# Kernel optimization log

Hardware: AMD Instinct MI355X
Metric: run time of the kernel (lower is better)

## Reference

```python
import jax, jax.numpy as jnp
import numpy as np

B, T, E = 4, 2048, 1024
H, KV = 16, 4          # query heads, key/value heads
D = E // H             # head_dim = 64
G = H // KV            # query heads per kv head = 4
NEG = -1e9


def setup_inputs() -> dict:
    key = jax.random.key(0)
    ks = jax.random.split(key, 6)
    hidden_states = jax.random.normal(ks[0], (B, T, E), dtype=jnp.float32)
    # additive causal mask [B, 1, T, T]
    causal = jnp.where(jnp.tril(jnp.ones((T, T), dtype=bool)), 0.0, NEG).astype(jnp.float32)
    attention_mask = jnp.broadcast_to(causal[None, None], (B, 1, T, T))
    s = 0.02
    Wq = jax.random.normal(ks[1], (E, E), dtype=jnp.float32) * s
    Wk = jax.random.normal(ks[2], (E, KV * D), dtype=jnp.float32) * s
    Wv = jax.random.normal(ks[3], (E, KV * D), dtype=jnp.float32) * s
    Wo = jax.random.normal(ks[4], (E, E), dtype=jnp.float32) * s
    bq = jnp.zeros((E,), jnp.float32)
    bk = jnp.zeros((KV * D,), jnp.float32)
    bv = jnp.zeros((KV * D,), jnp.float32)
    bo = jnp.zeros((E,), jnp.float32)
    return {"hidden_states": hidden_states, "attention_mask": attention_mask,
            "Wq": Wq, "bq": bq, "Wk": Wk, "bk": bk, "Wv": Wv, "bv": bv,
            "Wo": Wo, "bo": bo}


def reference(hidden_states, attention_mask, Wq, bq, Wk, bk, Wv, bv, Wo, bo):
    b, t, e = hidden_states.shape
    scaling = D ** -0.5
    # projections (torch Linear: x @ W + b with W stored [in, out])
    q = (hidden_states @ Wq + bq) * scaling           # [b, t, E]
    k = hidden_states @ Wk + bk                        # [b, t, KV*D]
    v = hidden_states @ Wv + bv
    # [b, KV, G, t, D] for q; [b, KV, t, D] for k/v (GQA grouping == repeat_kv math)
    q = q.reshape(b, t, KV, G, D).transpose(0, 2, 3, 1, 4)
    k = k.reshape(b, t, KV, D).transpose(0, 2, 1, 3)
    v = v.reshape(b, t, KV, D).transpose(0, 2, 1, 3)
    scores = jnp.einsum('bkgsd,bktd->bkgst', q, k)     # [b, KV, G, t, t]
    scores = scores + attention_mask[:, :, None, :, :]  # broadcast [b,1,1,t,t]
    w = jax.nn.softmax(scores, axis=-1)
    out = jnp.einsum('bkgst,bktd->bkgsd', w, v)        # [b, KV, G, t, D]
    out = out.transpose(0, 3, 1, 2, 4).reshape(b, t, e)  # heads back to embed
    return out @ Wo + bo
```

## Files before the change

kernel.cpp:

```cpp
#include <hip/hip_runtime.h>

typedef __bf16 bf16;
typedef __attribute__((ext_vector_type(8))) __bf16 bf16x8;
typedef __attribute__((ext_vector_type(4))) __bf16 bf16x4;
typedef __attribute__((ext_vector_type(4))) float f32x4;

#define B_ 4
#define T_ 2048
#define E_ 1024
#define H_ 16
#define KV_ 4
#define D_ 64
#define KVD_ 256
#define QKVS_ 1536
#define M_ 8192

#define MASK_NEG (-3.0e4f)
#define QSCALE (0.125f * 1.4426950408889634f)

__device__ inline bf16x8 load8(const bf16* p) { return *(const bf16x8*)p; }
__device__ inline bf16x8 load8(const float* p) {
  f32x4 a = *(const f32x4*)p;
  f32x4 b = *(const f32x4*)(p + 4);
  bf16x8 r;
#pragma unroll
  for (int j = 0; j < 4; ++j) { r[j] = (bf16)a[j]; r[4 + j] = (bf16)b[j]; }
  return r;
}

__device__ inline void gload_lds16(const bf16* g, bf16* l) {
  __builtin_amdgcn_global_load_lds(
      (const __attribute__((address_space(1))) void*)g,
      (__attribute__((address_space(3))) void*)l, 16, 0, 0);
}

__global__ __launch_bounds__(256) void prep_k(const float* __restrict__ hidden,
                                              bf16* __restrict__ Hb,
                                              const float* __restrict__ Wq,
                                              const float* __restrict__ Wk,
                                              const float* __restrict__ Wv,
                                              const float* __restrict__ Wo,
                                              bf16* __restrict__ WqkvT,
                                              bf16* __restrict__ WoT) {
  const int z = blockIdx.z;
  if (z >= 4) {
    size_t lin = (size_t)blockIdx.x + 32 * blockIdx.y + 1024 * (z - 4);
    size_t i = lin * 2048 + (size_t)threadIdx.x * 8;
    *(bf16x8*)(Hb + i) = load8(hidden + i);
    return;
  }
  const float* W;
  bf16* WT;
  int N;
  if (z == 0) { W = Wq; WT = WqkvT; N = 1024; }
  else if (z == 1) { W = Wo; WT = WoT; N = 1024; }
  else if (z == 2) { if (blockIdx.y >= 8) return; W = Wk; WT = WqkvT + 1024 * 1024; N = 256; }
  else { if (blockIdx.y >= 8) return; W = Wv; WT = WqkvT + 1280 * 1024; N = 256; }

  __shared__ bf16 tile[32][33];
  int k0 = blockIdx.x * 32, n0 = blockIdx.y * 32;
  int tr = threadIdx.x >> 5;
  int tc = threadIdx.x & 31;
#pragma unroll
  for (int i = 0; i < 32; i += 8)
    tile[tr + i][tc] = (bf16)W[(size_t)(k0 + tr + i) * N + n0 + tc];
  __syncthreads();
#pragma unroll
  for (int i = 0; i < 32; i += 8)
    WT[(size_t)(n0 + tr + i) * 1024 + k0 + tc] = tile[tc][tr + i];
}

__global__ __launch_bounds__(256) void vtrans_k(const bf16* __restrict__ src,
                                                bf16* __restrict__ dst) {
  __shared__ bf16 tile[32][33];
  int r0 = blockIdx.x * 32;
  int c0 = blockIdx.y * 32;
  int tr = threadIdx.x >> 5, tc = threadIdx.x & 31;
#pragma unroll
  for (int i = 0; i < 32; i += 8)
    tile[tr + i][tc] = src[(size_t)(r0 + tr + i) * QKVS_ + 1280 + c0 + tc];
  __syncthreads();
#pragma unroll
  for (int i = 0; i < 32; i += 8) {
    int c = c0 + tr + i;
    int r = r0 + tc;
    dst[(size_t)((r >> 11) * KVD_ + c) * T_ + (r & (T_ - 1))] = tile[tc][tr + i];
  }
}

__global__ __launch_bounds__(256) void qkv_gemm_k(const bf16* __restrict__ A,
                                                  const bf16* __restrict__ WT,
                                                  const float* __restrict__ bq,
                                                  const float* __restrict__ bk,
                                                  const float* __restrict__ bv,
                                                  bf16* __restrict__ C) {
  const int K = E_;
  const int m0 = blockIdx.x * 128;
  const int n0 = blockIdx.y * 128;
  const int tid = threadIdx.x;
  const int wave = tid >> 6;
  const int lane = tid & 63;
  const int wr = wave >> 1;
  const int wc = wave & 1;
  const int fr = lane & 15;
  const int quad = lane >> 4;

  __shared__ bf16 sA[128][32];
  __shared__ bf16 sB[128][32];

  f32x4 acc[4][4] = {};

  const int ldr = lane >> 2;
  const int ldk = (lane & 3) * 8;
  const bf16* Ag0 = A + (size_t)(m0 + wave * 32 + ldr) * K + ldk;
  const bf16* Ag1 = Ag0 + (size_t)16 * K;
  const bf16* Bg0 = WT + (size_t)(n0 + wave * 32 + ldr) * K + ldk;
  const bf16* Bg1 = Bg0 + (size_t)16 * K;
  bf16* sA0 = &sA[wave * 32][0];
  bf16* sA1 = &sA[wave * 32 + 16][0];
  bf16* sB0 = &sB[wave * 32][0];
  bf16* sB1 = &sB[wave * 32 + 16][0];

  for (int k0 = 0; k0 < K; k0 += 32) {
    gload_lds16(Ag0 + k0, sA0);
    gload_lds16(Ag1 + k0, sA1);
    gload_lds16(Bg0 + k0, sB0);
    gload_lds16(Bg1 + k0, sB1);
    __syncthreads();

    bf16x8 af[4], bfr[4];
#pragma unroll
    for (int m = 0; m < 4; ++m)
      af[m] = *(const bf16x8*)(&sA[wr * 64 + m * 16 + fr][quad * 8]);
#pragma unroll
    for (int n = 0; n < 4; ++n)
      bfr[n] = *(const bf16x8*)(&sB[wc * 64 + n * 16 + fr][quad * 8]);
#pragma unroll
    for (int m = 0; m < 4; ++m)
#pragma unroll
      for (int n = 0; n < 4; ++n)
        acc[m][n] = __builtin_amdgcn_mfma_f32_16x16x32_bf16(af[m], bfr[n], acc[m][n], 0, 0, 0);
    __syncthreads();
  }

#pragma unroll
  for (int n = 0; n < 4; ++n) {
    int col = n0 + wc * 64 + n * 16 + fr;
    float bias, sc;
    if (col < 1024) { bias = bq[col]; sc = QSCALE; }
    else if (col < 1280) { bias = bk[col - 1024]; sc = 1.f; }
    else { bias = bv[col - 1280]; sc = 1.f; }
#pragma unroll
    for (int m = 0; m < 4; ++m) {
#pragma unroll
      for (int i = 0; i < 4; ++i) {
        int row = m0 + wr * 64 + m * 16 + quad * 4 + i;
        C[(size_t)row * QKVS_ + col] = (bf16)((acc[m][n][i] + bias) * sc);
      }
    }
  }
}

__global__ __launch_bounds__(256) void gemm128_k(const bf16* __restrict__ A,
                                                 const bf16* __restrict__ WT,
                                                 const float* __restrict__ bias,
                                                 float* __restrict__ C,
                                                 int M, int N, int K) {
  const int m0 = blockIdx.x * 128;
  const int n0 = blockIdx.y * 128;
  const int tid = threadIdx.x;
  const int wave = tid >> 6;
  const int lane = tid & 63;
  const int wr = wave >> 1;
  const int wc = wave & 1;
  const int fr = lane & 15;
  const int quad = lane >> 4;

  __shared__ bf16 sA[128][32];
  __shared__ bf16 sB[128][32];

  f32x4 acc[4][4] = {};

  const int ldr = lane >> 2;
  const int ldk = (lane & 3) * 8;
  const bf16* Ag0 = A + (size_t)(m0 + wave * 32 + ldr) * K + ldk;
  const bf16* Ag1 = Ag0 + (size_t)16 * K;
  const bf16* Bg0 = WT + (size_t)(n0 + wave * 32 + ldr) * K + ldk;
  const bf16* Bg1 = Bg0 + (size_t)16 * K;
  bf16* sA0 = &sA[wave * 32][0];
  bf16* sA1 = &sA[wave * 32 + 16][0];
  bf16* sB0 = &sB[wave * 32][0];
  bf16* sB1 = &sB[wave * 32 + 16][0];

  for (int k0 = 0; k0 < K; k0 += 32) {
    gload_lds16(Ag0 + k0, sA0);
    gload_lds16(Ag1 + k0, sA1);
    gload_lds16(Bg0 + k0, sB0);
    gload_lds16(Bg1 + k0, sB1);
    __syncthreads();

    bf16x8 af[4], bfr[4];
#pragma unroll
    for (int m = 0; m < 4; ++m)
      af[m] = *(const bf16x8*)(&sA[wr * 64 + m * 16 + fr][quad * 8]);
#pragma unroll
    for (int n = 0; n < 4; ++n)
      bfr[n] = *(const bf16x8*)(&sB[wc * 64 + n * 16 + fr][quad * 8]);
#pragma unroll
    for (int m = 0; m < 4; ++m)
#pragma unroll
      for (int n = 0; n < 4; ++n)
        acc[m][n] = __builtin_amdgcn_mfma_f32_16x16x32_bf16(af[m], bfr[n], acc[m][n], 0, 0, 0);
    __syncthreads();
  }

#pragma unroll
  for (int n = 0; n < 4; ++n) {
    int col = n0 + wc * 64 + n * 16 + fr;
    float bv = bias[col];
#pragma unroll
    for (int m = 0; m < 4; ++m) {
#pragma unroll
      for (int i = 0; i < 4; ++i) {
        int row = m0 + wr * 64 + m * 16 + quad * 4 + i;
        C[(size_t)row * N + col] = (acc[m][n][i] + bv);
      }
    }
  }
}

__global__ __launch_bounds__(256) void attn_k(const bf16* __restrict__ QKVg,
                                              const bf16* __restrict__ VTg,
                                              bf16* __restrict__ Og) {
  const int jp = blockIdx.x;
  const int h = blockIdx.y;
  const int b = blockIdx.z;
  const int kv = h >> 2;
  const int tid = threadIdx.x;
  const int wave = tid >> 6;
  const int lane = tid & 63;
  const int fr = lane & 15;
  const int quad = lane >> 4;

  __shared__ bf16 Ks[64][72];
  __shared__ bf16 Vt[64][72];
  __shared__ bf16 Pt[64][72];

  const int skey = tid & 63;
  const int sdc = (tid >> 6) * 16;
  const int svd = tid >> 2;
  const int svk = (tid & 3) * 16;
  const bf16* kbase = QKVg + (size_t)(b * T_ + skey) * QKVS_ + 1024 + kv * 64 + sdc;
  const bf16* vbase = VTg + (size_t)((b * KV_ + kv) * D_ + svd) * T_ + svk;

  for (int ph = 0; ph < 2; ++ph) {
    const int qb = ph ? (31 - jp) : jp;

    bf16x8 qa0, qa1;
    {
      const bf16* qsrc = QKVg + (size_t)(b * T_ + qb * 64 + wave * 16 + fr) * QKVS_ + h * 64 + quad * 8;
      qa0 = *(const bf16x8*)(qsrc);
      qa1 = *(const bf16x8*)(qsrc + 32);
    }

    f32x4 Oacc[4] = {};
    float l_run = 0.f;

    bf16x8 k0p, k1p, v0p, v1p;
    k0p = *(const bf16x8*)(kbase);
    k1p = *(const bf16x8*)(kbase + 8);
    v0p = *(const bf16x8*)(vbase);
    v1p = *(const bf16x8*)(vbase + 8);

    for (int kb = 0; kb <= qb; ++kb) {
      *(bf16x8*)(&Ks[skey][sdc]) = k0p;
      *(bf16x8*)(&Ks[skey][sdc + 8]) = k1p;
      *(bf16x8*)(&Vt[svd][svk]) = v0p;
      *(bf16x8*)(&Vt[svd][svk + 8]) = v1p;
      __syncthreads();

      if (kb < qb) {
        const bf16* kp = kbase + (size_t)(kb + 1) * 64 * QKVS_;
        const bf16* vp = vbase + (size_t)(kb + 1) * 64;
        k0p = *(const bf16x8*)(kp);
        k1p = *(const bf16x8*)(kp + 8);
        v0p = *(const bf16x8*)(vp);
        v1p = *(const bf16x8*)(vp + 8);
      } else if (ph == 0) {
        k0p = *(const bf16x8*)(kbase);
        k1p = *(const bf16x8*)(kbase + 8);
        v0p = *(const bf16x8*)(vbase);
        v1p = *(const bf16x8*)(vbase + 8);
      }

      f32x4 S[4] = {};
      __builtin_amdgcn_s_setprio(1);
#pragma unroll
      for (int nt = 0; nt < 4; ++nt) {
        bf16x8 kf0 = *(const bf16x8*)(&Ks[nt * 16 + fr][quad * 8]);
        bf16x8 kf1 = *(const bf16x8*)(&Ks[nt * 16 + fr][32 + quad * 8]);
        S[nt] = __builtin_amdgcn_mfma_f32_16x16x32_bf16(kf0, qa0, S[nt], 0, 0, 0);
        S[nt] = __builtin_amdgcn_mfma_f32_16x16x32_bf16(kf1, qa1, S[nt], 0, 0, 0);
      }
      __builtin_amdgcn_s_setprio(0);

      if (kb == qb) {
        const int ql = wave * 16 + fr;
#pragma unroll
        for (int nt = 0; nt < 4; ++nt)
#pragma unroll
          for (int i = 0; i < 4; ++i)
            if (nt * 16 + quad * 4 + i > ql) S[nt][i] = MASK_NEG;
      }

      float ps = 0.f;
#pragma unroll
      for (int nt = 0; nt < 4; ++nt)
#pragma unroll
        for (int i = 0; i < 4; ++i) {
          float p = exp2f(S[nt][i]);
          S[nt][i] = p;
          ps += p;
        }
      ps += __shfl_xor(ps, 16, 64);
      ps += __shfl_xor(ps, 32, 64);
      l_run += ps;

#pragma unroll
      for (int nt = 0; nt < 4; ++nt) {
        bf16x4 w;
#pragma unroll
        for (int i = 0; i < 4; ++i) w[i] = (bf16)S[nt][i];
        *(bf16x4*)(&Pt[wave * 16 + fr][nt * 16 + quad * 4]) = w;
      }
      __threadfence_block();

      bf16x8 pb0 = *(const bf16x8*)(&Pt[wave * 16 + fr][quad * 8]);
      bf16x8 pb1 = *(const bf16x8*)(&Pt[wave * 16 + fr][32 + quad * 8]);
      __builtin_amdgcn_s_setprio(1);
#pragma unroll
      for (int dt = 0; dt < 4; ++dt) {
        bf16x8 vf0 = *(const bf16x8*)(&Vt[dt * 16 + fr][quad * 8]);
        bf16x8 vf1 = *(const bf16x8*)(&Vt[dt * 16 + fr][32 + quad * 8]);
        Oacc[dt] = __builtin_amdgcn_mfma_f32_16x16x32_bf16(vf0, pb0, Oacc[dt], 0, 0, 0);
        Oacc[dt] = __builtin_amdgcn_mfma_f32_16x16x32_bf16(vf1, pb1, Oacc[dt], 0, 0, 0);
      }
      __builtin_amdgcn_s_setprio(0);
      __syncthreads();
    }

    {
      float inv = 1.f / fmaxf(l_run, 1e-30f);
      bf16* dst = Og + (size_t)(b * T_ + qb * 64 + wave * 16 + fr) * E_ + h * 64;
#pragma unroll
      for (int dt = 0; dt < 4; ++dt) {
        bf16x4 o;
#pragma unroll
        for (int i = 0; i < 4; ++i) o[i] = (bf16)(Oacc[dt][i] * inv);
        *(bf16x4*)(dst + dt * 16 + quad * 4) = o;
      }
    }
  }
}

extern "C" void kernel_launch(void* const* d_in, const int* in_sizes, int n_in,
                              void* d_out, int out_size, void* d_ws, size_t ws_size,
                              hipStream_t stream) {
  (void)in_sizes; (void)n_in; (void)out_size; (void)ws_size;
  const float* hidden = (const float*)d_in[0];
  const float* Wq = (const float*)d_in[2];
  const float* bq = (const float*)d_in[3];
  const float* Wk = (const float*)d_in[4];
  const float* bk = (const float*)d_in[5];
  const float* Wv = (const float*)d_in[6];
  const float* bv = (const float*)d_in[7];
  const float* Wo = (const float*)d_in[8];
  const float* bo = (const float*)d_in[9];
  float* out = (float*)d_out;

  char* ws = (char*)d_ws;
  bf16* WqkvT = (bf16*)(ws);
  bf16* WoT   = (bf16*)(ws + (3u << 20));
  bf16* QKVb  = (bf16*)(ws + (5u << 20));
  bf16* Hb    = (bf16*)(ws + (29u << 20));
  bf16* Ab    = (bf16*)(ws + (29u << 20));
  bf16* VbT   = (bf16*)(ws + (45u << 20));

  prep_k<<<dim3(32, 32, 8), 256, 0, stream>>>(hidden, Hb, Wq, Wk, Wv, Wo, WqkvT, WoT);

  qkv_gemm_k<<<dim3(64, 12), 256, 0, stream>>>(Hb, WqkvT, bq, bk, bv, QKVb);

  vtrans_k<<<dim3(256, 8), 256, 0, stream>>>(QKVb, VbT);

  attn_k<<<dim3(16, 16, 4), 256, 0, stream>>>(QKVb, VbT, Ab);

  gemm128_k<<<dim3(64, 8), 256, 0, stream>>>(Ab, WoT, bo, out, M_, E_, E_);
}
```

Baseline: 278.4 us.

## Use two waves per attention block, each handling 32 query rows

The attention kernel drops from four waves of 256 threads to two waves of 128 threads, and each wave now processes two 16-row query subtiles. Every K and V fragment read from shared memory is reused across twice as many MFMAs, which cuts LDS read traffic and barrier participants per block. Each thread now stages 32 elements of K and V instead of 16, and register use rises from doubled accumulators and Q fragments. Fewer waves per block may lower the latency hiding available within a block.

```diff
diff --git a/kernel.cpp b/kernel.cpp
--- a/kernel.cpp
+++ b/kernel.cpp
@@ -229,7 +229,7 @@
   }
 }
 
-__global__ __launch_bounds__(256) void attn_k(const bf16* __restrict__ QKVg,
+__global__ __launch_bounds__(128) void attn_k(const bf16* __restrict__ QKVg,
                                               const bf16* __restrict__ VTg,
                                               bf16* __restrict__ Og) {
   const int jp = blockIdx.x;
@@ -247,36 +247,45 @@
   __shared__ bf16 Pt[64][72];
 
   const int skey = tid & 63;
-  const int sdc = (tid >> 6) * 16;
-  const int svd = tid >> 2;
-  const int svk = (tid & 3) * 16;
-  const bf16* kbase = QKVg + (size_t)(b * T_ + skey) * QKVS_ + 1024 + kv * 64 + sdc;
-  const bf16* vbase = VTg + (size_t)((b * KV_ + kv) * D_ + svd) * T_ + svk;
+  const int sseg = (tid >> 6) * 32;
+  const bf16* kbase = QKVg + (size_t)(b * T_ + skey) * QKVS_ + 1024 + kv * 64 + sseg;
+  const bf16* vbase = VTg + (size_t)((b * KV_ + kv) * D_ + skey) * T_ + sseg;
 
   for (int ph = 0; ph < 2; ++ph) {
     const int qb = ph ? (31 - jp) : jp;
 
-    bf16x8 qa0, qa1;
+    bf16x8 qa0, qa1, qc0, qc1;
     {
-      const bf16* qsrc = QKVg + (size_t)(b * T_ + qb * 64 + wave * 16 + fr) * QKVS_ + h * 64 + quad * 8;
+      const bf16* qsrc = QKVg + (size_t)(b * T_ + qb * 64 + wave * 32 + fr) * QKVS_ + h * 64 + quad * 8;
       qa0 = *(const bf16x8*)(qsrc);
       qa1 = *(const bf16x8*)(qsrc + 32);
+      const bf16* qsrc2 = qsrc + (size_t)16 * QKVS_;
+      qc0 = *(const bf16x8*)(qsrc2);
+      qc1 = *(const bf16x8*)(qsrc2 + 32);
     }
 
-    f32x4 Oacc[4] = {};
-    float l_run = 0.f;
-
-    bf16x8 k0p, k1p, v0p, v1p;
+    f32x4 O0[4] = {}, O1[4] = {};
+    float l0 = 0.f, l1 = 0.f;
+
+    bf16x8 k0p, k1p, k2p, k3p, v0p, v1p, v2p, v3p;
     k0p = *(const bf16x8*)(kbase);
     k1p = *(const bf16x8*)(kbase + 8);
+    k2p = *(const bf16x8*)(kbase + 16);
+    k3p = *(const bf16x8*)(kbase + 24);
     v0p = *(const bf16x8*)(vbase);
     v1p = *(const bf16x8*)(vbase + 8);
+    v2p = *(const bf16x8*)(vbase + 16);
+    v3p = *(const bf16x8*)(vbase + 24);
 
     for (int kb = 0; kb <= qb; ++kb) {
-      *(bf16x8*)(&Ks[skey][sdc]) = k0p;
-      *(bf16x8*)(&Ks[skey][sdc + 8]) = k1p;
-      *(bf16x8*)(&Vt[svd][svk]) = v0p;
-      *(bf16x8*)(&Vt[svd][svk + 8]) = v1p;
+      *(bf16x8*)(&Ks[skey][sseg]) = k0p;
+      *(bf16x8*)(&Ks[skey][sseg + 8]) = k1p;
+      *(bf16x8*)(&Ks[skey][sseg + 16]) = k2p;
+      *(bf16x8*)(&Ks[skey][sseg + 24]) = k3p;
+      *(bf16x8*)(&Vt[skey][sseg]) = v0p;
+      *(bf16x8*)(&Vt[skey][sseg + 8]) = v1p;
+      *(bf16x8*)(&Vt[skey][sseg + 16]) = v2p;
+      *(bf16x8*)(&Vt[skey][sseg + 24]) = v3p;
       __syncthreads();
 
       if (kb < qb) {
@@ -284,80 +293,111 @@
         const bf16* vp = vbase + (size_t)(kb + 1) * 64;
         k0p = *(const bf16x8*)(kp);
         k1p = *(const bf16x8*)(kp + 8);
+        k2p = *(const bf16x8*)(kp + 16);
+        k3p = *(const bf16x8*)(kp + 24);
         v0p = *(const bf16x8*)(vp);
         v1p = *(const bf16x8*)(vp + 8);
+        v2p = *(const bf16x8*)(vp + 16);
+        v3p = *(const bf16x8*)(vp + 24);
       } else if (ph == 0) {
         k0p = *(const bf16x8*)(kbase);
         k1p = *(const bf16x8*)(kbase + 8);
+        k2p = *(const bf16x8*)(kbase + 16);
+        k3p = *(const bf16x8*)(kbase + 24);
         v0p = *(const bf16x8*)(vbase);
         v1p = *(const bf16x8*)(vbase + 8);
-      }
-
-      f32x4 S[4] = {};
+        v2p = *(const bf16x8*)(vbase + 16);
+        v3p = *(const bf16x8*)(vbase + 24);
+      }
+
+      f32x4 S0[4] = {}, S1[4] = {};
       __builtin_amdgcn_s_setprio(1);
 #pragma unroll
       for (int nt = 0; nt < 4; ++nt) {
         bf16x8 kf0 = *(const bf16x8*)(&Ks[nt * 16 + fr][quad * 8]);
         bf16x8 kf1 = *(const bf16x8*)(&Ks[nt * 16 + fr][32 + quad * 8]);
-        S[nt] = __builtin_amdgcn_mfma_f32_16x16x32_bf16(kf0, qa0, S[nt], 0, 0, 0);
-        S[nt] = __builtin_amdgcn_mfma_f32_16x16x32_bf16(kf1, qa1, S[nt], 0, 0, 0);
+        S0[nt] = __builtin_amdgcn_mfma_f32_16x16x32_bf16(kf0, qa0, S0[nt], 0, 0, 0);
+        S0[nt] = __builtin_amdgcn_mfma_f32_16x16x32_bf16(kf1, qa1, S0[nt], 0, 0, 0);
+        S1[nt] = __builtin_amdgcn_mfma_f32_16x16x32_bf16(kf0, qc0, S1[nt], 0, 0, 0);
+        S1[nt] = __builtin_amdgcn_mfma_f32_16x16x32_bf16(kf1, qc1, S1[nt], 0, 0, 0);
       }
       __builtin_amdgcn_s_setprio(0);
 
       if (kb == qb) {
-        const int ql = wave * 16 + fr;
+        const int ql0 = wave * 32 + fr;
+        const int ql1 = ql0 + 16;
 #pragma unroll
         for (int nt = 0; nt < 4; ++nt)
 #pragma unroll
-          for (int i = 0; i < 4; ++i)
-            if (nt * 16 + quad * 4 + i > ql) S[nt][i] = MASK_NEG;
-      }
-
-      float ps = 0.f;
+          for (int i = 0; i < 4; ++i) {
+            int key = nt * 16 + quad * 4 + i;
+            if (key > ql0) S0[nt][i] = MASK_NEG;
+            if (key > ql1) S1[nt][i] = MASK_NEG;
+          }
+      }
+
+      float ps0 = 0.f, ps1 = 0.f;
 #pragma unroll
       for (int nt = 0; nt < 4; ++nt)
 #pragma unroll
         for (int i = 0; i < 4; ++i) {
-          float p = exp2f(S[nt][i]);
-          S[nt][i] = p;
-          ps += p;
+          float p0 = exp2f(S0[nt][i]);
+          float p1 = exp2f(S1[nt][i]);
+          S0[nt][i] = p0;
+          S1[nt][i] = p1;
+          ps0 += p0;
+          ps1 += p1;
         }
-      ps += __shfl_xor(ps, 16, 64);
-      ps += __shfl_xor(ps, 32, 64);
-      l_run += ps;
+      ps0 += __shfl_xor(ps0, 16, 64);
+      ps0 += __shfl_xor(ps0, 32, 64);
+      ps1 += __shfl_xor(ps1, 16, 64);
+      ps1 += __shfl_xor(ps1, 32, 64);
+      l0 += ps0;
+      l1 += ps1;
 
 #pragma unroll
       for (int nt = 0; nt < 4; ++nt) {
-        bf16x4 w;
-#pragma unroll
-        for (int i = 0; i < 4; ++i) w[i] = (bf16)S[nt][i];
-        *(bf16x4*)(&Pt[wave * 16 + fr][nt * 16 + quad * 4]) = w;
+        bf16x4 w0, w1;
+#pragma unroll
+        for (int i = 0; i < 4; ++i) { w0[i] = (bf16)S0[nt][i]; w1[i] = (bf16)S1[nt][i]; }
+        *(bf16x4*)(&Pt[wave * 32 + fr][nt * 16 + quad * 4]) = w0;
+        *(bf16x4*)(&Pt[wave * 32 + 16 + fr][nt * 16 + quad * 4]) = w1;
       }
       __threadfence_block();
 
-      bf16x8 pb0 = *(const bf16x8*)(&Pt[wave * 16 + fr][quad * 8]);
-      bf16x8 pb1 = *(const bf16x8*)(&Pt[wave * 16 + fr][32 + quad * 8]);
+      bf16x8 pb00 = *(const bf16x8*)(&Pt[wave * 32 + fr][quad * 8]);
+      bf16x8 pb01 = *(const bf16x8*)(&Pt[wave * 32 + fr][32 + quad * 8]);
+      bf16x8 pb10 = *(const bf16x8*)(&Pt[wave * 32 + 16 + fr][quad * 8]);
+      bf16x8 pb11 = *(const bf16x8*)(&Pt[wave * 32 + 16 + fr][32 + quad * 8]);
       __builtin_amdgcn_s_setprio(1);
 #pragma unroll
       for (int dt = 0; dt < 4; ++dt) {
         bf16x8 vf0 = *(const bf16x8*)(&Vt[dt * 16 + fr][quad * 8]);
         bf16x8 vf1 = *(const bf16x8*)(&Vt[dt * 16 + fr][32 + quad * 8]);
-        Oacc[dt] = __builtin_amdgcn_mfma_f32_16x16x32_bf16(vf0, pb0, Oacc[dt], 0, 0, 0);
-        Oacc[dt] = __builtin_amdgcn_mfma_f32_16x16x32_bf16(vf1, pb1, Oacc[dt], 0, 0, 0);
+        O0[dt] = __builtin_amdgcn_mfma_f32_16x16x32_bf16(vf0, pb00, O0[dt], 0, 0, 0);
+        O0[dt] = __builtin_amdgcn_mfma_f32_16x16x32_bf16(vf1, pb01, O0[dt], 0, 0, 0);
+        O1[dt] = __builtin_amdgcn_mfma_f32_16x16x32_bf16(vf0, pb10, O1[dt], 0, 0, 0);
+        O1[dt] = __builtin_amdgcn_mfma_f32_16x16x32_bf16(vf1, pb11, O1[dt], 0, 0, 0);
       }
       __builtin_amdgcn_s_setprio(0);
       __syncthreads();
     }
 
     {
-      float inv = 1.f / fmaxf(l_run, 1e-30f);
-      bf16* dst = Og + (size_t)(b * T_ + qb * 64 + wave * 16 + fr) * E_ + h * 64;
+      float inv0 = 1.f / fmaxf(l0, 1e-30f);
+      float inv1 = 1.f / fmaxf(l1, 1e-30f);
+      bf16* dst0 = Og + (size_t)(b * T_ + qb * 64 + wave * 32 + fr) * E_ + h * 64;
+      bf16* dst1 = dst0 + (size_t)16 * E_;
 #pragma unroll
       for (int dt = 0; dt < 4; ++dt) {
-        bf16x4 o;
-#pragma unroll
-        for (int i = 0; i < 4; ++i) o[i] = (bf16)(Oacc[dt][i] * inv);
-        *(bf16x4*)(dst + dt * 16 + quad * 4) = o;
+        bf16x4 o0, o1;
+#pragma unroll
+        for (int i = 0; i < 4; ++i) {
+          o0[i] = (bf16)(O0[dt][i] * inv0);
+          o1[i] = (bf16)(O1[dt][i] * inv1);
+        }
+        *(bf16x4*)(dst0 + dt * 16 + quad * 4) = o0;
+        *(bf16x4*)(dst1 + dt * 16 + quad * 4) = o1;
       }
     }
   }
@@ -392,7 +432,7 @@
 
   vtrans_k<<<dim3(256, 8), 256, 0, stream>>>(QKVb, VbT);
 
-  attn_k<<<dim3(16, 16, 4), 256, 0, stream>>>(QKVb, VbT, Ab);
+  attn_k<<<dim3(16, 16, 4), 128, 0, stream>>>(QKVb, VbT, Ab);
 
   gemm128_k<<<dim3(64, 8), 256, 0, stream>>>(Ab, WoT, bo, out, M_, E_, E_);
 }
```

Measured after the change: 286.3 us. 2.9% more time.

## Double-buffer LDS tiles in QKV and output projection GEMMs

Applied to the files above, without the earlier changes.

Both GEMM kernels now hold two LDS buffers for the A and B tiles. They prefetch the next K-slice with gload_lds while MFMAs run on the current slice, and they drop the barrier that used to sit between load and compute. The aim is to hide global-to-LDS latency behind matrix math. In exchange the kernels use twice the shared memory per block, which may lower occupancy, and they rely on the trailing __syncthreads to wait for the async loads.

```diff
diff --git a/kernel.cpp b/kernel.cpp
--- a/kernel.cpp
+++ b/kernel.cpp
@@ -105,8 +105,8 @@
   const int fr = lane & 15;
   const int quad = lane >> 4;
 
-  __shared__ bf16 sA[128][32];
-  __shared__ bf16 sB[128][32];
+  __shared__ bf16 sA[2][128][32];
+  __shared__ bf16 sB[2][128][32];
 
   f32x4 acc[4][4] = {};
 
@@ -116,25 +116,30 @@
   const bf16* Ag1 = Ag0 + (size_t)16 * K;
   const bf16* Bg0 = WT + (size_t)(n0 + wave * 32 + ldr) * K + ldk;
   const bf16* Bg1 = Bg0 + (size_t)16 * K;
-  bf16* sA0 = &sA[wave * 32][0];
-  bf16* sA1 = &sA[wave * 32 + 16][0];
-  bf16* sB0 = &sB[wave * 32][0];
-  bf16* sB1 = &sB[wave * 32 + 16][0];
+
+  gload_lds16(Ag0, &sA[0][wave * 32][0]);
+  gload_lds16(Ag1, &sA[0][wave * 32 + 16][0]);
+  gload_lds16(Bg0, &sB[0][wave * 32][0]);
+  gload_lds16(Bg1, &sB[0][wave * 32 + 16][0]);
+  __syncthreads();
 
   for (int k0 = 0; k0 < K; k0 += 32) {
-    gload_lds16(Ag0 + k0, sA0);
-    gload_lds16(Ag1 + k0, sA1);
-    gload_lds16(Bg0 + k0, sB0);
-    gload_lds16(Bg1 + k0, sB1);
-    __syncthreads();
+    const int cur = (k0 >> 5) & 1;
+    if (k0 + 32 < K) {
+      const int nxt = cur ^ 1;
+      gload_lds16(Ag0 + k0 + 32, &sA[nxt][wave * 32][0]);
+      gload_lds16(Ag1 + k0 + 32, &sA[nxt][wave * 32 + 16][0]);
+      gload_lds16(Bg0 + k0 + 32, &sB[nxt][wave * 32][0]);
+      gload_lds16(Bg1 + k0 + 32, &sB[nxt][wave * 32 + 16][0]);
+    }
 
     bf16x8 af[4], bfr[4];
 #pragma unroll
     for (int m = 0; m < 4; ++m)
-      af[m] = *(const bf16x8*)(&sA[wr * 64 + m * 16 + fr][quad * 8]);
+      af[m] = *(const bf16x8*)(&sA[cur][wr * 64 + m * 16 + fr][quad * 8]);
 #pragma unroll
     for (int n = 0; n < 4; ++n)
-      bfr[n] = *(const bf16x8*)(&sB[wc * 64 + n * 16 + fr][quad * 8]);
+      bfr[n] = *(const bf16x8*)(&sB[cur][wc * 64 + n * 16 + fr][quad * 8]);
 #pragma unroll
     for (int m = 0; m < 4; ++m)
 #pragma unroll
@@ -176,8 +181,8 @@
   const int fr = lane & 15;
   const int quad = lane >> 4;
 
-  __shared__ bf16 sA[128][32];
-  __shared__ bf16 sB[128][32];
+  __shared__ bf16 sA[2][128][32];
+  __shared__ bf16 sB[2][128][32];
 
   f32x4 acc[4][4] = {};
 
@@ -187,25 +192,30 @@
   const bf16* Ag1 = Ag0 + (size_t)16 * K;
   const bf16* Bg0 = WT + (size_t)(n0 + wave * 32 + ldr) * K + ldk;
   const bf16* Bg1 = Bg0 + (size_t)16 * K;
-  bf16* sA0 = &sA[wave * 32][0];
-  bf16* sA1 = &sA[wave * 32 + 16][0];
-  bf16* sB0 = &sB[wave * 32][0];
-  bf16* sB1 = &sB[wave * 32 + 16][0];
+
+  gload_lds16(Ag0, &sA[0][wave * 32][0]);
+  gload_lds16(Ag1, &sA[0][wave * 32 + 16][0]);
+  gload_lds16(Bg0, &sB[0][wave * 32][0]);
+  gload_lds16(Bg1, &sB[0][wave * 32 + 16][0]);
+  __syncthreads();
 
   for (int k0 = 0; k0 < K; k0 += 32) {
-    gload_lds16(Ag0 + k0, sA0);
-    gload_lds16(Ag1 + k0, sA1);
-    gload_lds16(Bg0 + k0, sB0);
-    gload_lds16(Bg1 + k0, sB1);
-    __syncthreads();
+    const int cur = (k0 >> 5) & 1;
+    if (k0 + 32 < K) {
+      const int nxt = cur ^ 1;
+      gload_lds16(Ag0 + k0 + 32, &sA[nxt][wave * 32][0]);
+      gload_lds16(Ag1 + k0 + 32, &sA[nxt][wave * 32 + 16][0]);
+      gload_lds16(Bg0 + k0 + 32, &sB[nxt][wave * 32][0]);
+      gload_lds16(Bg1 + k0 + 32, &sB[nxt][wave * 32 + 16][0]);
+    }
 
     bf16x8 af[4], bfr[4];
 #pragma unroll
     for (int m = 0; m < 4; ++m)
-      af[m] = *(const bf16x8*)(&sA[wr * 64 + m * 16 + fr][quad * 8]);
+      af[m] = *(const bf16x8*)(&sA[cur][wr * 64 + m * 16 + fr][quad * 8]);
 #pragma unroll
     for (int n = 0; n < 4; ++n)
-      bfr[n] = *(const bf16x8*)(&sB[wc * 64 + n * 16 + fr][quad * 8]);
+      bfr[n] = *(const bf16x8*)(&sB[cur][wc * 64 + n * 16 + fr][quad * 8]);
 #pragma unroll
     for (int m = 0; m < 4; ++m)
 #pragma unroll
```

After: 274.8 us. About the same (-1.3%).
